# Kernel optimization log

Measured on AMD Instinct MI355X. Metric: run time of the kernel, lower is better.

Reference implementation:

```python
import jax, jax.numpy as jnp
import numpy as np

N_NODES = 50000
N_EDGES = 400000
IN_DIM = 128
HID_DIM = 128
OUT_DIM = 128


def setup_inputs() -> dict:
    key = jax.random.key(0)
    k_x, k_e, k_w1, k_b1, k_w2, k_b2 = jax.random.split(key, 6)
    x = jax.random.normal(k_x, (N_NODES, IN_DIM), dtype=jnp.float32)
    edge_index = jax.random.randint(k_e, (2, N_EDGES), 0, N_NODES, dtype=jnp.int64)
    # nn.Linear-style params: W is [out, in], kaiming-uniform-ish init
    lim1 = 1.0 / np.sqrt(IN_DIM)
    lim2 = 1.0 / np.sqrt(HID_DIM)
    W1 = jax.random.uniform(k_w1, (HID_DIM, IN_DIM), jnp.float32, -lim1, lim1)
    b1 = jax.random.uniform(k_b1, (HID_DIM,), jnp.float32, -lim1, lim1)
    W2 = jax.random.uniform(k_w2, (OUT_DIM, HID_DIM), jnp.float32, -lim2, lim2)
    b2 = jax.random.uniform(k_b2, (OUT_DIM,), jnp.float32, -lim2, lim2)
    return {"x": x, "edge_index": edge_index, "W1": W1, "b1": b1, "W2": W2, "b2": b2}


def reference(x, edge_index, W1, b1, W2, b2):
    # h = relu(fc1(x));  dropout in eval mode -> identity
    h = jax.nn.relu(x @ W1.T + b1)                      # [N, hid]
    src, dst = edge_index[0], edge_index[1]
    # gather messages from src, scatter-add (mean) into dst
    agg = jax.ops.segment_sum(h[src], dst, num_segments=N_NODES)      # [N, hid]
    deg = jax.ops.segment_sum(jnp.ones_like(dst, dtype=h.dtype), dst,
                              num_segments=N_NODES)                   # [N]
    deg = jnp.maximum(deg, 1.0)
    agg = agg / deg[:, None]
    # residual add + fc2
    return (agg + h) @ W2.T + b2                        # [N, out]
```

## Files before the change

kernel.cpp:

```cpp
#include <hip/hip_runtime.h>

#define N_NODES 50000
#define N_EDGES 400000
#define DIM 128
#define N_SCAN_BLK ((N_NODES + 255) / 256)
#define BUCKET_BLK ((N_EDGES + 255) / 256)
#define FC1_BLK ((N_NODES + 63) / 64)

typedef unsigned short u16;
typedef unsigned int   u32;
typedef __bf16 v8bf  __attribute__((ext_vector_type(8)));
typedef float  f32x4 __attribute__((ext_vector_type(4)));
typedef u16    u16x8 __attribute__((ext_vector_type(8)));

union BF8 { u16x8 u; v8bf b; };

__device__ __forceinline__ float bf2f(u16 u) {
    union { u32 i; float f; } v; v.i = ((u32)u) << 16; return v.f;
}
__device__ __forceinline__ u16 f2bf(float f) {
    union { float f; u32 i; } v; v.f = f; u32 u = v.i;
    return (u16)((u + 0x7FFFu + ((u >> 16) & 1u)) >> 16);
}

__global__ __launch_bounds__(256) void count_cast_kernel(
    const int* __restrict__ edst, int* __restrict__ counts,
    const float* __restrict__ W1, const float* __restrict__ W2,
    u16* __restrict__ Wb1, u16* __restrict__ Wb2)
{
    int bid = blockIdx.x;
    if (bid < BUCKET_BLK) {
        int e = bid * 256 + threadIdx.x;
        if (e >= N_EDGES) return;
        int dst = edst[e];
        if ((unsigned)dst >= N_NODES) return;
        atomicAdd(&counts[dst], 1);
    } else {
        int i = (bid - BUCKET_BLK) * 256 + threadIdx.x;
        if (i < DIM * DIM) {
            Wb1[i] = f2bf(W1[i]);
            Wb2[i] = f2bf(W2[i]);
        }
    }
}

__global__ __launch_bounds__(256) void scan_blocks_kernel(
    const int* __restrict__ counts, int* __restrict__ row_ptr,
    int* __restrict__ bsum)
{
    __shared__ int tmp[256];
    const int t = threadIdx.x;
    const int i = blockIdx.x * 256 + t;
    int v = (i < N_NODES) ? counts[i] : 0;
    tmp[t] = v;
    __syncthreads();
#pragma unroll
    for (int ofs = 1; ofs < 256; ofs <<= 1) {
        int add = (t >= ofs) ? tmp[t - ofs] : 0;
        __syncthreads();
        tmp[t] += add;
        __syncthreads();
    }
    if (i < N_NODES) row_ptr[i] = tmp[t] - v;
    if (t == 255) bsum[blockIdx.x] = tmp[255];
}

__global__ __launch_bounds__(256) void scan_fixup2_kernel(
    const int* __restrict__ bsum, int* __restrict__ row_ptr,
    int* __restrict__ cursor)
{
    __shared__ int tmp[256];
    __shared__ int ex[256];
    const int t = threadIdx.x;
    int v = (t < N_SCAN_BLK) ? bsum[t] : 0;
    tmp[t] = v;
    __syncthreads();
#pragma unroll
    for (int ofs = 1; ofs < 256; ofs <<= 1) {
        int add = (t >= ofs) ? tmp[t - ofs] : 0;
        __syncthreads();
        tmp[t] += add;
        __syncthreads();
    }
    ex[t] = tmp[t] - v;
    __syncthreads();

    int boff = ex[blockIdx.x];
    int i = blockIdx.x * 256 + t;
    if (i < N_NODES) {
        int r = row_ptr[i] + boff;
        row_ptr[i] = r;
        cursor[i]  = r;
    }
    if (i == 0) row_ptr[N_NODES] = N_EDGES;
}

__global__ __launch_bounds__(256, 3) void bucket_fc1_kernel(
    const int* __restrict__ esrc, const int* __restrict__ edst,
    int* __restrict__ cursor, int* __restrict__ esorted,
    const float* __restrict__ x, const u16* __restrict__ Wb,
    const float* __restrict__ b, u16* __restrict__ h)
{
    __shared__ u16 xs[64 * 136];
    const int bid = blockIdx.x;

    if (bid < BUCKET_BLK) {
        int e = bid * 256 + threadIdx.x;
        if (e < N_EDGES) {
            int src = esrc[e], dst = edst[e];
            if ((unsigned)src < N_NODES && (unsigned)dst < N_NODES) {
                int pos = atomicAdd(&cursor[dst], 1);
                esorted[pos] = src;
            }
        }
        return;
    }

    const int t = threadIdx.x;
    const int wave = t >> 6, lane = t & 63, quad = lane >> 4, l15 = lane & 15;
    const int ch = wave >> 1, rh = wave & 1;
    const int row0 = (bid - BUCKET_BLK) * 64;

    BF8 barr[4][4];
#pragma unroll
    for (int ct = 0; ct < 4; ++ct)
#pragma unroll
        for (int ks = 0; ks < 4; ++ks)
            barr[ct][ks].u = *(const u16x8*)(
                Wb + (size_t)(ch * 64 + ct * 16 + l15) * DIM + ks * 32 + quad * 8);

    {
        int srow = t >> 2, k0 = (t & 3) * 32;
        int grow = row0 + srow; if (grow >= N_NODES) grow = N_NODES - 1;
        const float* xp = x + (size_t)grow * DIM + k0;
#pragma unroll
        for (int j = 0; j < 4; ++j) {
            float4 f0 = *(const float4*)(xp + j * 8);
            float4 f1 = *(const float4*)(xp + j * 8 + 4);
            u16x8 p;
            p[0] = f2bf(f0.x); p[1] = f2bf(f0.y); p[2] = f2bf(f0.z); p[3] = f2bf(f0.w);
            p[4] = f2bf(f1.x); p[5] = f2bf(f1.y); p[6] = f2bf(f1.z); p[7] = f2bf(f1.w);
            *(u16x8*)&xs[srow * 136 + k0 + j * 8] = p;
        }
    }

    f32x4 acc[2][4];
#pragma unroll
    for (int ct = 0; ct < 4; ++ct) {
        float bv = b[ch * 64 + ct * 16 + l15];
        acc[0][ct] = (f32x4){bv, bv, bv, bv};
        acc[1][ct] = (f32x4){bv, bv, bv, bv};
    }
    __syncthreads();

#pragma unroll
    for (int ks = 0; ks < 4; ++ks) {
        BF8 a0, a1;
        a0.u = *(const u16x8*)&xs[(rh * 32 +  0 + l15) * 136 + ks * 32 + quad * 8];
        a1.u = *(const u16x8*)&xs[(rh * 32 + 16 + l15) * 136 + ks * 32 + quad * 8];
#pragma unroll
        for (int ct = 0; ct < 4; ++ct) {
            acc[0][ct] = __builtin_amdgcn_mfma_f32_16x16x32_bf16(
                a0.b, barr[ct][ks].b, acc[0][ct], 0, 0, 0);
            acc[1][ct] = __builtin_amdgcn_mfma_f32_16x16x32_bf16(
                a1.b, barr[ct][ks].b, acc[1][ct], 0, 0, 0);
        }
    }

#pragma unroll
    for (int rt = 0; rt < 2; ++rt)
#pragma unroll
        for (int i = 0; i < 4; ++i) {
            int row = row0 + rh * 32 + rt * 16 + quad * 4 + i;
            if (row < N_NODES) {
#pragma unroll
                for (int ct = 0; ct < 4; ++ct) {
                    int col = ch * 64 + ct * 16 + l15;
                    h[(size_t)row * DIM + col] = f2bf(fmaxf(acc[rt][ct][i], 0.f));
                }
            }
        }
}

__global__ __launch_bounds__(256) void aggregate_kernel(
    const int* __restrict__ row_ptr, const int* __restrict__ esorted,
    const u16* __restrict__ h, u16* __restrict__ z)
{
    const int wave = threadIdx.x >> 6;
    const int lane = threadIdx.x & 63;
    const int n = blockIdx.x * 4 + wave;
    if (n >= N_NODES) return;

    const int start = row_ptr[n];
    const int end   = row_ptr[n + 1];

    float a0 = 0.f, a1 = 0.f;
    int e = start;
    for (; e + 8 <= end; e += 8) {
        int s0 = esorted[e + 0], s1 = esorted[e + 1];
        int s2 = esorted[e + 2], s3 = esorted[e + 3];
        int s4 = esorted[e + 4], s5 = esorted[e + 5];
        int s6 = esorted[e + 6], s7 = esorted[e + 7];
        u32 v0 = *(const u32*)(h + (size_t)s0 * DIM + lane * 2);
        u32 v1 = *(const u32*)(h + (size_t)s1 * DIM + lane * 2);
        u32 v2 = *(const u32*)(h + (size_t)s2 * DIM + lane * 2);
        u32 v3 = *(const u32*)(h + (size_t)s3 * DIM + lane * 2);
        u32 v4 = *(const u32*)(h + (size_t)s4 * DIM + lane * 2);
        u32 v5 = *(const u32*)(h + (size_t)s5 * DIM + lane * 2);
        u32 v6 = *(const u32*)(h + (size_t)s6 * DIM + lane * 2);
        u32 v7 = *(const u32*)(h + (size_t)s7 * DIM + lane * 2);
        a0 += bf2f((u16)v0); a1 += bf2f((u16)(v0 >> 16));
        a0 += bf2f((u16)v1); a1 += bf2f((u16)(v1 >> 16));
        a0 += bf2f((u16)v2); a1 += bf2f((u16)(v2 >> 16));
        a0 += bf2f((u16)v3); a1 += bf2f((u16)(v3 >> 16));
        a0 += bf2f((u16)v4); a1 += bf2f((u16)(v4 >> 16));
        a0 += bf2f((u16)v5); a1 += bf2f((u16)(v5 >> 16));
        a0 += bf2f((u16)v6); a1 += bf2f((u16)(v6 >> 16));
        a0 += bf2f((u16)v7); a1 += bf2f((u16)(v7 >> 16));
    }
    for (; e + 4 <= end; e += 4) {
        int s0 = esorted[e + 0], s1 = esorted[e + 1];
        int s2 = esorted[e + 2], s3 = esorted[e + 3];
        u32 v0 = *(const u32*)(h + (size_t)s0 * DIM + lane * 2);
        u32 v1 = *(const u32*)(h + (size_t)s1 * DIM + lane * 2);
        u32 v2 = *(const u32*)(h + (size_t)s2 * DIM + lane * 2);
        u32 v3 = *(const u32*)(h + (size_t)s3 * DIM + lane * 2);
        a0 += bf2f((u16)v0); a1 += bf2f((u16)(v0 >> 16));
        a0 += bf2f((u16)v1); a1 += bf2f((u16)(v1 >> 16));
        a0 += bf2f((u16)v2); a1 += bf2f((u16)(v2 >> 16));
        a0 += bf2f((u16)v3); a1 += bf2f((u16)(v3 >> 16));
    }
    for (; e < end; ++e) {
        u32 v = *(const u32*)(h + (size_t)esorted[e] * DIM + lane * 2);
        a0 += bf2f((u16)v); a1 += bf2f((u16)(v >> 16));
    }

    int deg = end - start;
    float inv = (deg > 0) ? 1.f / (float)deg : 1.f;
    u32 r = *(const u32*)(h + (size_t)n * DIM + lane * 2);
    float z0 = a0 * inv + bf2f((u16)r);
    float z1 = a1 * inv + bf2f((u16)(r >> 16));
    u32 p = (u32)f2bf(z0) | ((u32)f2bf(z1) << 16);
    *(u32*)(z + (size_t)n * DIM + lane * 2) = p;
}

__global__ __launch_bounds__(256, 3) void fc2_mfma(
    const u16* __restrict__ z, const u16* __restrict__ Wb,
    const float* __restrict__ b, float* __restrict__ out)
{
    __shared__ u16 xs[64 * 136];
    const int t = threadIdx.x;
    const int wave = t >> 6, lane = t & 63, quad = lane >> 4, l15 = lane & 15;
    const int ch = wave >> 1, rh = wave & 1;
    const int row0 = blockIdx.x * 64;

    BF8 barr[4][4];
#pragma unroll
    for (int ct = 0; ct < 4; ++ct)
#pragma unroll
        for (int ks = 0; ks < 4; ++ks)
            barr[ct][ks].u = *(const u16x8*)(
                Wb + (size_t)(ch * 64 + ct * 16 + l15) * DIM + ks * 32 + quad * 8);

    {
        int srow = t >> 1, k0 = (t & 1) * 64;
        int grow = row0 + srow; if (grow >= N_NODES) grow = N_NODES - 1;
        const u16* zp = z + (size_t)grow * DIM + k0;
#pragma unroll
        for (int j = 0; j < 8; ++j)
            *(u16x8*)&xs[srow * 136 + k0 + j * 8] = *(const u16x8*)(zp + j * 8);
    }

    f32x4 acc[2][4];
#pragma unroll
    for (int ct = 0; ct < 4; ++ct) {
        float bv = b[ch * 64 + ct * 16 + l15];
        acc[0][ct] = (f32x4){bv, bv, bv, bv};
        acc[1][ct] = (f32x4){bv, bv, bv, bv};
    }
    __syncthreads();

#pragma unroll
    for (int ks = 0; ks < 4; ++ks) {
        BF8 a0, a1;
        a0.u = *(const u16x8*)&xs[(rh * 32 +  0 + l15) * 136 + ks * 32 + quad * 8];
        a1.u = *(const u16x8*)&xs[(rh * 32 + 16 + l15) * 136 + ks * 32 + quad * 8];
#pragma unroll
        for (int ct = 0; ct < 4; ++ct) {
            acc[0][ct] = __builtin_amdgcn_mfma_f32_16x16x32_bf16(
                a0.b, barr[ct][ks].b, acc[0][ct], 0, 0, 0);
            acc[1][ct] = __builtin_amdgcn_mfma_f32_16x16x32_bf16(
                a1.b, barr[ct][ks].b, acc[1][ct], 0, 0, 0);
        }
    }

#pragma unroll
    for (int rt = 0; rt < 2; ++rt)
#pragma unroll
        for (int i = 0; i < 4; ++i) {
            int row = row0 + rh * 32 + rt * 16 + quad * 4 + i;
            if (row < N_NODES) {
#pragma unroll
                for (int ct = 0; ct < 4; ++ct) {
                    int col = ch * 64 + ct * 16 + l15;
                    out[(size_t)row * DIM + col] = acc[rt][ct][i];
                }
            }
        }
}

extern "C" void kernel_launch(void* const* d_in, const int* in_sizes, int n_in,
                              void* d_out, int out_size, void* d_ws, size_t ws_size,
                              hipStream_t stream)
{
    const float* x  = (const float*)d_in[0];
    const int*   ei = (const int*)d_in[1];
    const float* W1 = (const float*)d_in[2];
    const float* b1 = (const float*)d_in[3];
    const float* W2 = (const float*)d_in[4];
    const float* b2 = (const float*)d_in[5];
    float* out = (float*)d_out;

    const int* esrc = ei;
    const int* edst = ei + N_EDGES;

    char* ws = (char*)d_ws;
    size_t off = 0;
    u16* h        = (u16*)(ws + off); off += (size_t)N_NODES * DIM * 2;
    u16* z        = (u16*)(ws + off); off += (size_t)N_NODES * DIM * 2;
    u16* Wb1      = (u16*)(ws + off); off += (size_t)DIM * DIM * 2;
    u16* Wb2      = (u16*)(ws + off); off += (size_t)DIM * DIM * 2;
    int* counts   = (int*)(ws + off); off += (size_t)N_NODES * 4;
    int* row_ptr  = (int*)(ws + off); off += (size_t)(N_NODES + 1) * 4;
    int* cursor   = (int*)(ws + off); off += (size_t)N_NODES * 4;
    int* esorted  = (int*)(ws + off); off += (size_t)N_EDGES * 4;
    int* bsum     = (int*)(ws + off); off += (size_t)N_SCAN_BLK * 4;

    hipMemsetAsync(counts, 0, (size_t)N_NODES * 4, stream);
    count_cast_kernel<<<BUCKET_BLK + 64, 256, 0, stream>>>(
        edst, counts, W1, W2, Wb1, Wb2);
    scan_blocks_kernel<<<N_SCAN_BLK, 256, 0, stream>>>(counts, row_ptr, bsum);
    scan_fixup2_kernel<<<N_SCAN_BLK, 256, 0, stream>>>(bsum, row_ptr, cursor);
    bucket_fc1_kernel<<<BUCKET_BLK + FC1_BLK, 256, 0, stream>>>(
        esrc, edst, cursor, esorted, x, Wb1, b1, h);
    aggregate_kernel<<<(N_NODES + 3) / 4, 256, 0, stream>>>(
        row_ptr, esorted, h, z);
    fc2_mfma<<<(N_NODES + 63) / 64, 256, 0, stream>>>(z, Wb2, b2, out);
}
```

Measured before the change: 177.6 us.

## Fuse whole GNN pipeline into one cooperative persistent kernel with grid syncs

```diff
diff --git a/kernel.cpp b/kernel.cpp
--- a/kernel.cpp
+++ b/kernel.cpp
@@ -1,4 +1,5 @@
 #include <hip/hip_runtime.h>
+#include <hip/hip_cooperative_groups.h>
 
 #define N_NODES 50000
 #define N_EDGES 400000
@@ -21,6 +22,267 @@
 __device__ __forceinline__ u16 f2bf(float f) {
     union { float f; u32 i; } v; v.f = f; u32 u = v.i;
     return (u16)((u + 0x7FFFu + ((u >> 16) & 1u)) >> 16);
+}
+
+__global__ __launch_bounds__(256, 3) void mega_kernel(
+    const float* __restrict__ x,
+    const int* __restrict__ esrc, const int* __restrict__ edst,
+    const float* __restrict__ W1, const float* __restrict__ b1,
+    const float* __restrict__ W2, const float* __restrict__ b2,
+    float* __restrict__ out,
+    u16* __restrict__ h, u16* __restrict__ Wb1, u16* __restrict__ Wb2,
+    int* __restrict__ counts, int* __restrict__ row_ptr,
+    int* __restrict__ cursor, int* __restrict__ esorted,
+    int* __restrict__ gcursor)
+{
+    cooperative_groups::grid_group grid = cooperative_groups::this_grid();
+    __shared__ __align__(16) char smem[64 * 136 * 2];
+    u16* xs = (u16*)smem;
+
+    const int nb   = (int)gridDim.x;
+    const int bid  = (int)blockIdx.x;
+    const int t    = (int)threadIdx.x;
+    const int gtid = bid * 256 + t;
+    const int gsz  = nb * 256;
+
+    for (int i = gtid; i < N_NODES; i += gsz) counts[i] = 0;
+    for (int i = gtid; i < DIM * DIM; i += gsz) {
+        Wb1[i] = f2bf(W1[i]);
+        Wb2[i] = f2bf(W2[i]);
+    }
+    if (gtid == 0) *gcursor = 0;
+    grid.sync();
+
+    for (int e = gtid; e < N_EDGES; e += gsz) {
+        int dst = edst[e];
+        int src = esrc[e];
+        if ((unsigned)dst < N_NODES && (unsigned)src < N_NODES)
+            atomicAdd(&counts[dst], 1);
+    }
+    grid.sync();
+
+    {
+        int* tmp   = (int*)smem;
+        int* sbase = tmp + 256;
+        for (int sb = bid; sb < N_SCAN_BLK; sb += nb) {
+            int i = sb * 256 + t;
+            int v = (i < N_NODES) ? counts[i] : 0;
+            tmp[t] = v;
+            __syncthreads();
+#pragma unroll
+            for (int ofs = 1; ofs < 256; ofs <<= 1) {
+                int add = (t >= ofs) ? tmp[t - ofs] : 0;
+                __syncthreads();
+                tmp[t] += add;
+                __syncthreads();
+            }
+            int ex = tmp[t] - v;
+            if (t == 255) *sbase = atomicAdd(gcursor, tmp[255]);
+            __syncthreads();
+            if (i < N_NODES) {
+                int r = *sbase + ex;
+                row_ptr[i] = r;
+                cursor[i]  = r;
+            }
+            __syncthreads();
+        }
+    }
+    grid.sync();
+
+    for (int e = gtid; e < N_EDGES; e += gsz) {
+        int src = esrc[e], dst = edst[e];
+        if ((unsigned)src < N_NODES && (unsigned)dst < N_NODES) {
+            int pos = atomicAdd(&cursor[dst], 1);
+            esorted[pos] = src;
+        }
+    }
+
+    {
+        const int wave = t >> 6, lane = t & 63, quad = lane >> 4, l15 = lane & 15;
+        const int ch = wave >> 1, rh = wave & 1;
+
+        BF8 barr[4][4];
+#pragma unroll
+        for (int ct = 0; ct < 4; ++ct)
+#pragma unroll
+            for (int ks = 0; ks < 4; ++ks)
+                barr[ct][ks].u = *(const u16x8*)(
+                    Wb1 + (size_t)(ch * 64 + ct * 16 + l15) * DIM + ks * 32 + quad * 8);
+        float bv[4];
+#pragma unroll
+        for (int ct = 0; ct < 4; ++ct) bv[ct] = b1[ch * 64 + ct * 16 + l15];
+
+        for (int tile = bid; tile < FC1_BLK; tile += nb) {
+            const int row0 = tile * 64;
+            {
+                int srow = t >> 2, k0 = (t & 3) * 32;
+                int grow = row0 + srow; if (grow >= N_NODES) grow = N_NODES - 1;
+                const float* xp = x + (size_t)grow * DIM + k0;
+#pragma unroll
+                for (int j = 0; j < 4; ++j) {
+                    float4 f0 = *(const float4*)(xp + j * 8);
+                    float4 f1 = *(const float4*)(xp + j * 8 + 4);
+                    u16x8 p;
+                    p[0] = f2bf(f0.x); p[1] = f2bf(f0.y); p[2] = f2bf(f0.z); p[3] = f2bf(f0.w);
+                    p[4] = f2bf(f1.x); p[5] = f2bf(f1.y); p[6] = f2bf(f1.z); p[7] = f2bf(f1.w);
+                    *(u16x8*)&xs[srow * 136 + k0 + j * 8] = p;
+                }
+            }
+            f32x4 acc[2][4];
+#pragma unroll
+            for (int ct = 0; ct < 4; ++ct) {
+                acc[0][ct] = (f32x4){bv[ct], bv[ct], bv[ct], bv[ct]};
+                acc[1][ct] = (f32x4){bv[ct], bv[ct], bv[ct], bv[ct]};
+            }
+            __syncthreads();
+#pragma unroll
+            for (int ks = 0; ks < 4; ++ks) {
+                BF8 a0, a1;
+                a0.u = *(const u16x8*)&xs[(rh * 32 +  0 + l15) * 136 + ks * 32 + quad * 8];
+                a1.u = *(const u16x8*)&xs[(rh * 32 + 16 + l15) * 136 + ks * 32 + quad * 8];
+#pragma unroll
+                for (int ct = 0; ct < 4; ++ct) {
+                    acc[0][ct] = __builtin_amdgcn_mfma_f32_16x16x32_bf16(
+                        a0.b, barr[ct][ks].b, acc[0][ct], 0, 0, 0);
+                    acc[1][ct] = __builtin_amdgcn_mfma_f32_16x16x32_bf16(
+                        a1.b, barr[ct][ks].b, acc[1][ct], 0, 0, 0);
+                }
+            }
+#pragma unroll
+            for (int rt = 0; rt < 2; ++rt)
+#pragma unroll
+                for (int i = 0; i < 4; ++i) {
+                    int row = row0 + rh * 32 + rt * 16 + quad * 4 + i;
+                    if (row < N_NODES) {
+#pragma unroll
+                        for (int ct = 0; ct < 4; ++ct) {
+                            int col = ch * 64 + ct * 16 + l15;
+                            h[(size_t)row * DIM + col] = f2bf(fmaxf(acc[rt][ct][i], 0.f));
+                        }
+                    }
+                }
+            __syncthreads();
+        }
+    }
+    grid.sync();
+
+    {
+        const int wv = t >> 6, ln = t & 63;
+        const int quad = ln >> 4, l15 = ln & 15;
+        const int ch = wv >> 1, rh = wv & 1;
+
+        BF8 barr[4][4];
+#pragma unroll
+        for (int ct = 0; ct < 4; ++ct)
+#pragma unroll
+            for (int ks = 0; ks < 4; ++ks)
+                barr[ct][ks].u = *(const u16x8*)(
+                    Wb2 + (size_t)(ch * 64 + ct * 16 + l15) * DIM + ks * 32 + quad * 8);
+        float bv[4];
+#pragma unroll
+        for (int ct = 0; ct < 4; ++ct) bv[ct] = b2[ch * 64 + ct * 16 + l15];
+
+        for (int tile = bid; tile < FC1_BLK; tile += nb) {
+            const int row0 = tile * 64;
+
+            int nidx = row0 + wv * 16 + (ln & 15);
+            int myStart = 0, myDeg = 0;
+            if (nidx < N_NODES) { myStart = row_ptr[nidx]; myDeg = counts[nidx]; }
+
+#pragma unroll 1
+            for (int j = 0; j < 16; ++j) {
+                const int s = wv * 16 + j;
+                const int n = row0 + s;
+                const int start = __shfl(myStart, j, 64);
+                const int deg   = __shfl(myDeg,   j, 64);
+                u32 pack = 0;
+                if (n < N_NODES) {
+                    const int end = start + deg;
+                    float a0 = 0.f, a1 = 0.f;
+                    int e = start;
+                    for (; e + 8 <= end; e += 8) {
+                        int s0 = esorted[e + 0], s1 = esorted[e + 1];
+                        int s2 = esorted[e + 2], s3 = esorted[e + 3];
+                        int s4 = esorted[e + 4], s5 = esorted[e + 5];
+                        int s6 = esorted[e + 6], s7 = esorted[e + 7];
+                        u32 v0 = *(const u32*)(h + (size_t)s0 * DIM + ln * 2);
+                        u32 v1 = *(const u32*)(h + (size_t)s1 * DIM + ln * 2);
+                        u32 v2 = *(const u32*)(h + (size_t)s2 * DIM + ln * 2);
+                        u32 v3 = *(const u32*)(h + (size_t)s3 * DIM + ln * 2);
+                        u32 v4 = *(const u32*)(h + (size_t)s4 * DIM + ln * 2);
+                        u32 v5 = *(const u32*)(h + (size_t)s5 * DIM + ln * 2);
+                        u32 v6 = *(const u32*)(h + (size_t)s6 * DIM + ln * 2);
+                        u32 v7 = *(const u32*)(h + (size_t)s7 * DIM + ln * 2);
+                        a0 += bf2f((u16)v0); a1 += bf2f((u16)(v0 >> 16));
+                        a0 += bf2f((u16)v1); a1 += bf2f((u16)(v1 >> 16));
+                        a0 += bf2f((u16)v2); a1 += bf2f((u16)(v2 >> 16));
+                        a0 += bf2f((u16)v3); a1 += bf2f((u16)(v3 >> 16));
+                        a0 += bf2f((u16)v4); a1 += bf2f((u16)(v4 >> 16));
+                        a0 += bf2f((u16)v5); a1 += bf2f((u16)(v5 >> 16));
+                        a0 += bf2f((u16)v6); a1 += bf2f((u16)(v6 >> 16));
+                        a0 += bf2f((u16)v7); a1 += bf2f((u16)(v7 >> 16));
+                    }
+                    for (; e + 4 <= end; e += 4) {
+                        int s0 = esorted[e + 0], s1 = esorted[e + 1];
+                        int s2 = esorted[e + 2], s3 = esorted[e + 3];
+                        u32 v0 = *(const u32*)(h + (size_t)s0 * DIM + ln * 2);
+                        u32 v1 = *(const u32*)(h + (size_t)s1 * DIM + ln * 2);
+                        u32 v2 = *(const u32*)(h + (size_t)s2 * DIM + ln * 2);
+                        u32 v3 = *(const u32*)(h + (size_t)s3 * DIM + ln * 2);
+                        a0 += bf2f((u16)v0); a1 += bf2f((u16)(v0 >> 16));
+                        a0 += bf2f((u16)v1); a1 += bf2f((u16)(v1 >> 16));
+                        a0 += bf2f((u16)v2); a1 += bf2f((u16)(v2 >> 16));
+                        a0 += bf2f((u16)v3); a1 += bf2f((u16)(v3 >> 16));
+                    }
+                    for (; e < end; ++e) {
+                        u32 v = *(const u32*)(h + (size_t)esorted[e] * DIM + ln * 2);
+                        a0 += bf2f((u16)v); a1 += bf2f((u16)(v >> 16));
+                    }
+                    u32 r = *(const u32*)(h + (size_t)n * DIM + ln * 2);
+                    float inv = (deg > 0) ? 1.f / (float)deg : 1.f;
+                    float z0 = a0 * inv + bf2f((u16)r);
+                    float z1 = a1 * inv + bf2f((u16)(r >> 16));
+                    pack = (u32)f2bf(z0) | ((u32)f2bf(z1) << 16);
+                }
+                *(u32*)&xs[s * 136 + ln * 2] = pack;
+            }
+            __syncthreads();
+
+            f32x4 acc[2][4];
+#pragma unroll
+            for (int ct = 0; ct < 4; ++ct) {
+                acc[0][ct] = (f32x4){bv[ct], bv[ct], bv[ct], bv[ct]};
+                acc[1][ct] = (f32x4){bv[ct], bv[ct], bv[ct], bv[ct]};
+            }
+#pragma unroll
+            for (int ks = 0; ks < 4; ++ks) {
+                BF8 a0, a1;
+                a0.u = *(const u16x8*)&xs[(rh * 32 +  0 + l15) * 136 + ks * 32 + quad * 8];
+                a1.u = *(const u16x8*)&xs[(rh * 32 + 16 + l15) * 136 + ks * 32 + quad * 8];
+#pragma unroll
+                for (int ct = 0; ct < 4; ++ct) {
+                    acc[0][ct] = __builtin_amdgcn_mfma_f32_16x16x32_bf16(
+                        a0.b, barr[ct][ks].b, acc[0][ct], 0, 0, 0);
+                    acc[1][ct] = __builtin_amdgcn_mfma_f32_16x16x32_bf16(
+                        a1.b, barr[ct][ks].b, acc[1][ct], 0, 0, 0);
+                }
+            }
+#pragma unroll
+            for (int rt = 0; rt < 2; ++rt)
+#pragma unroll
+                for (int i = 0; i < 4; ++i) {
+                    int row = row0 + rh * 32 + rt * 16 + quad * 4 + i;
+                    if (row < N_NODES) {
+#pragma unroll
+                        for (int ct = 0; ct < 4; ++ct) {
+                            int col = ch * 64 + ct * 16 + l15;
+                            out[(size_t)row * DIM + col] = acc[rt][ct][i];
+                        }
+                    }
+                }
+            __syncthreads();
+        }
+    }
 }
 
 __global__ __launch_bounds__(256) void count_cast_kernel(
@@ -335,6 +597,33 @@
     int* cursor   = (int*)(ws + off); off += (size_t)N_NODES * 4;
     int* esorted  = (int*)(ws + off); off += (size_t)N_EDGES * 4;
     int* bsum     = (int*)(ws + off); off += (size_t)N_SCAN_BLK * 4;
+    int* gcursor  = (int*)(ws + off); off += 4;
+
+    static int coop_grid = -1;
+    if (coop_grid < 0) {
+        int nbpc = 0;
+        if (hipOccupancyMaxActiveBlocksPerMultiprocessor(&nbpc, mega_kernel, 256, 0)
+                != hipSuccess)
+            nbpc = 0;
+        if (nbpc > 0) {
+            long g = (long)nbpc * 256;
+            if (g > FC1_BLK) g = FC1_BLK;
+            coop_grid = (int)g;
+        } else {
+            coop_grid = 0;
+        }
+    }
+    if (coop_grid > 0) {
+        void* args[] = { (void*)&x, (void*)&esrc, (void*)&edst,
+                         (void*)&W1, (void*)&b1, (void*)&W2, (void*)&b2,
+                         (void*)&out, (void*)&h, (void*)&Wb1, (void*)&Wb2,
+                         (void*)&counts, (void*)&row_ptr, (void*)&cursor,
+                         (void*)&esorted, (void*)&gcursor };
+        if (hipLaunchCooperativeKernel(mega_kernel, dim3(coop_grid), dim3(256),
+                                       args, 0, stream) == hipSuccess)
+            return;
+        coop_grid = 0;
+    }
 
     hipMemsetAsync(counts, 0, (size_t)N_NODES * 4, stream);
     count_cast_kernel<<<BUCKET_BLK + 64, 256, 0, stream>>>(
```

Result: slower. 372.2 us (+109.6%).

## Replace CSR count/scan build with atomic linked-list adjacency per destination

Applied to the files above, without the earlier changes.

```diff
diff --git a/kernel.cpp b/kernel.cpp
--- a/kernel.cpp
+++ b/kernel.cpp
@@ -3,7 +3,6 @@
 #define N_NODES 50000
 #define N_EDGES 400000
 #define DIM 128
-#define N_SCAN_BLK ((N_NODES + 255) / 256)
 #define BUCKET_BLK ((N_EDGES + 255) / 256)
 #define FC1_BLK ((N_NODES + 63) / 64)
 
@@ -23,83 +22,11 @@
     return (u16)((u + 0x7FFFu + ((u >> 16) & 1u)) >> 16);
 }
 
-__global__ __launch_bounds__(256) void count_cast_kernel(
-    const int* __restrict__ edst, int* __restrict__ counts,
-    const float* __restrict__ W1, const float* __restrict__ W2,
-    u16* __restrict__ Wb1, u16* __restrict__ Wb2)
-{
-    int bid = blockIdx.x;
-    if (bid < BUCKET_BLK) {
-        int e = bid * 256 + threadIdx.x;
-        if (e >= N_EDGES) return;
-        int dst = edst[e];
-        if ((unsigned)dst >= N_NODES) return;
-        atomicAdd(&counts[dst], 1);
-    } else {
-        int i = (bid - BUCKET_BLK) * 256 + threadIdx.x;
-        if (i < DIM * DIM) {
-            Wb1[i] = f2bf(W1[i]);
-            Wb2[i] = f2bf(W2[i]);
-        }
-    }
-}
-
-__global__ __launch_bounds__(256) void scan_blocks_kernel(
-    const int* __restrict__ counts, int* __restrict__ row_ptr,
-    int* __restrict__ bsum)
-{
-    __shared__ int tmp[256];
-    const int t = threadIdx.x;
-    const int i = blockIdx.x * 256 + t;
-    int v = (i < N_NODES) ? counts[i] : 0;
-    tmp[t] = v;
-    __syncthreads();
-#pragma unroll
-    for (int ofs = 1; ofs < 256; ofs <<= 1) {
-        int add = (t >= ofs) ? tmp[t - ofs] : 0;
-        __syncthreads();
-        tmp[t] += add;
-        __syncthreads();
-    }
-    if (i < N_NODES) row_ptr[i] = tmp[t] - v;
-    if (t == 255) bsum[blockIdx.x] = tmp[255];
-}
-
-__global__ __launch_bounds__(256) void scan_fixup2_kernel(
-    const int* __restrict__ bsum, int* __restrict__ row_ptr,
-    int* __restrict__ cursor)
-{
-    __shared__ int tmp[256];
-    __shared__ int ex[256];
-    const int t = threadIdx.x;
-    int v = (t < N_SCAN_BLK) ? bsum[t] : 0;
-    tmp[t] = v;
-    __syncthreads();
-#pragma unroll
-    for (int ofs = 1; ofs < 256; ofs <<= 1) {
-        int add = (t >= ofs) ? tmp[t - ofs] : 0;
-        __syncthreads();
-        tmp[t] += add;
-        __syncthreads();
-    }
-    ex[t] = tmp[t] - v;
-    __syncthreads();
-
-    int boff = ex[blockIdx.x];
-    int i = blockIdx.x * 256 + t;
-    if (i < N_NODES) {
-        int r = row_ptr[i] + boff;
-        row_ptr[i] = r;
-        cursor[i]  = r;
-    }
-    if (i == 0) row_ptr[N_NODES] = N_EDGES;
-}
-
-__global__ __launch_bounds__(256, 3) void bucket_fc1_kernel(
+__global__ __launch_bounds__(256, 3) void build_fc1_kernel(
     const int* __restrict__ esrc, const int* __restrict__ edst,
-    int* __restrict__ cursor, int* __restrict__ esorted,
-    const float* __restrict__ x, const u16* __restrict__ Wb,
-    const float* __restrict__ b, u16* __restrict__ h)
+    int* __restrict__ head, int2* __restrict__ pairbuf,
+    const float* __restrict__ x, const float* __restrict__ W1,
+    const float* __restrict__ b1, u16* __restrict__ h)
 {
     __shared__ u16 xs[64 * 136];
     const int bid = blockIdx.x;
@@ -109,8 +36,8 @@
         if (e < N_EDGES) {
             int src = esrc[e], dst = edst[e];
             if ((unsigned)src < N_NODES && (unsigned)dst < N_NODES) {
-                int pos = atomicAdd(&cursor[dst], 1);
-                esorted[pos] = src;
+                int old = atomicExch(&head[dst], e);
+                pairbuf[e] = make_int2(old, src);
             }
         }
         return;
@@ -125,9 +52,16 @@
 #pragma unroll
     for (int ct = 0; ct < 4; ++ct)
 #pragma unroll
-        for (int ks = 0; ks < 4; ++ks)
-            barr[ct][ks].u = *(const u16x8*)(
-                Wb + (size_t)(ch * 64 + ct * 16 + l15) * DIM + ks * 32 + quad * 8);
+        for (int ks = 0; ks < 4; ++ks) {
+            const float* wp = W1 + (size_t)(ch * 64 + ct * 16 + l15) * DIM
+                                 + ks * 32 + quad * 8;
+            float4 f0 = *(const float4*)wp;
+            float4 f1 = *(const float4*)(wp + 4);
+            u16x8 p;
+            p[0] = f2bf(f0.x); p[1] = f2bf(f0.y); p[2] = f2bf(f0.z); p[3] = f2bf(f0.w);
+            p[4] = f2bf(f1.x); p[5] = f2bf(f1.y); p[6] = f2bf(f1.z); p[7] = f2bf(f1.w);
+            barr[ct][ks].u = p;
+        }
 
     {
         int srow = t >> 2, k0 = (t & 3) * 32;
@@ -147,7 +81,7 @@
     f32x4 acc[2][4];
 #pragma unroll
     for (int ct = 0; ct < 4; ++ct) {
-        float bv = b[ch * 64 + ct * 16 + l15];
+        float bv = b1[ch * 64 + ct * 16 + l15];
         acc[0][ct] = (f32x4){bv, bv, bv, bv};
         acc[1][ct] = (f32x4){bv, bv, bv, bv};
     }
@@ -183,7 +117,7 @@
 }
 
 __global__ __launch_bounds__(256) void aggregate_kernel(
-    const int* __restrict__ row_ptr, const int* __restrict__ esorted,
+    const int* __restrict__ head, const int2* __restrict__ pairbuf,
     const u16* __restrict__ h, u16* __restrict__ z)
 {
     const int wave = threadIdx.x >> 6;
@@ -191,62 +125,36 @@
     const int n = blockIdx.x * 4 + wave;
     if (n >= N_NODES) return;
 
-    const int start = row_ptr[n];
-    const int end   = row_ptr[n + 1];
-
     float a0 = 0.f, a1 = 0.f;
-    int e = start;
-    for (; e + 8 <= end; e += 8) {
-        int s0 = esorted[e + 0], s1 = esorted[e + 1];
-        int s2 = esorted[e + 2], s3 = esorted[e + 3];
-        int s4 = esorted[e + 4], s5 = esorted[e + 5];
-        int s6 = esorted[e + 6], s7 = esorted[e + 7];
-        u32 v0 = *(const u32*)(h + (size_t)s0 * DIM + lane * 2);
-        u32 v1 = *(const u32*)(h + (size_t)s1 * DIM + lane * 2);
-        u32 v2 = *(const u32*)(h + (size_t)s2 * DIM + lane * 2);
-        u32 v3 = *(const u32*)(h + (size_t)s3 * DIM + lane * 2);
-        u32 v4 = *(const u32*)(h + (size_t)s4 * DIM + lane * 2);
-        u32 v5 = *(const u32*)(h + (size_t)s5 * DIM + lane * 2);
-        u32 v6 = *(const u32*)(h + (size_t)s6 * DIM + lane * 2);
-        u32 v7 = *(const u32*)(h + (size_t)s7 * DIM + lane * 2);
-        a0 += bf2f((u16)v0); a1 += bf2f((u16)(v0 >> 16));
-        a0 += bf2f((u16)v1); a1 += bf2f((u16)(v1 >> 16));
-        a0 += bf2f((u16)v2); a1 += bf2f((u16)(v2 >> 16));
-        a0 += bf2f((u16)v3); a1 += bf2f((u16)(v3 >> 16));
-        a0 += bf2f((u16)v4); a1 += bf2f((u16)(v4 >> 16));
-        a0 += bf2f((u16)v5); a1 += bf2f((u16)(v5 >> 16));
-        a0 += bf2f((u16)v6); a1 += bf2f((u16)(v6 >> 16));
-        a0 += bf2f((u16)v7); a1 += bf2f((u16)(v7 >> 16));
-    }
-    for (; e + 4 <= end; e += 4) {
-        int s0 = esorted[e + 0], s1 = esorted[e + 1];
-        int s2 = esorted[e + 2], s3 = esorted[e + 3];
-        u32 v0 = *(const u32*)(h + (size_t)s0 * DIM + lane * 2);
-        u32 v1 = *(const u32*)(h + (size_t)s1 * DIM + lane * 2);
-        u32 v2 = *(const u32*)(h + (size_t)s2 * DIM + lane * 2);
-        u32 v3 = *(const u32*)(h + (size_t)s3 * DIM + lane * 2);
-        a0 += bf2f((u16)v0); a1 += bf2f((u16)(v0 >> 16));
-        a0 += bf2f((u16)v1); a1 += bf2f((u16)(v1 >> 16));
-        a0 += bf2f((u16)v2); a1 += bf2f((u16)(v2 >> 16));
-        a0 += bf2f((u16)v3); a1 += bf2f((u16)(v3 >> 16));
-    }
-    for (; e < end; ++e) {
-        u32 v = *(const u32*)(h + (size_t)esorted[e] * DIM + lane * 2);
-        a0 += bf2f((u16)v); a1 += bf2f((u16)(v >> 16));
-    }
-
-    int deg = end - start;
+    int deg = 0;
+    int e = head[n];
+    if (e >= 0) {
+        int2 p = pairbuf[e];
+        while (true) {
+            const int en  = p.x;
+            const int src = p.y;
+            u32 v = *(const u32*)(h + (size_t)src * DIM + lane * 2);
+            int2 pn;
+            const bool more = (en >= 0);
+            if (more) pn = pairbuf[en];
+            a0 += bf2f((u16)v); a1 += bf2f((u16)(v >> 16));
+            ++deg;
+            if (!more) break;
+            p = pn;
+        }
+    }
+
     float inv = (deg > 0) ? 1.f / (float)deg : 1.f;
     u32 r = *(const u32*)(h + (size_t)n * DIM + lane * 2);
     float z0 = a0 * inv + bf2f((u16)r);
     float z1 = a1 * inv + bf2f((u16)(r >> 16));
-    u32 p = (u32)f2bf(z0) | ((u32)f2bf(z1) << 16);
-    *(u32*)(z + (size_t)n * DIM + lane * 2) = p;
+    u32 pck = (u32)f2bf(z0) | ((u32)f2bf(z1) << 16);
+    *(u32*)(z + (size_t)n * DIM + lane * 2) = pck;
 }
 
 __global__ __launch_bounds__(256, 3) void fc2_mfma(
-    const u16* __restrict__ z, const u16* __restrict__ Wb,
-    const float* __restrict__ b, float* __restrict__ out)
+    const u16* __restrict__ z, const float* __restrict__ W2,
+    const float* __restrict__ b2, float* __restrict__ out)
 {
     __shared__ u16 xs[64 * 136];
     const int t = threadIdx.x;
@@ -258,9 +166,16 @@
 #pragma unroll
     for (int ct = 0; ct < 4; ++ct)
 #pragma unroll
-        for (int ks = 0; ks < 4; ++ks)
-            barr[ct][ks].u = *(const u16x8*)(
-                Wb + (size_t)(ch * 64 + ct * 16 + l15) * DIM + ks * 32 + quad * 8);
+        for (int ks = 0; ks < 4; ++ks) {
+            const float* wp = W2 + (size_t)(ch * 64 + ct * 16 + l15) * DIM
+                                 + ks * 32 + quad * 8;
+            float4 f0 = *(const float4*)wp;
+            float4 f1 = *(const float4*)(wp + 4);
+            u16x8 p;
+            p[0] = f2bf(f0.x); p[1] = f2bf(f0.y); p[2] = f2bf(f0.z); p[3] = f2bf(f0.w);
+            p[4] = f2bf(f1.x); p[5] = f2bf(f1.y); p[6] = f2bf(f1.z); p[7] = f2bf(f1.w);
+            barr[ct][ks].u = p;
+        }
 
     {
         int srow = t >> 1, k0 = (t & 1) * 64;
@@ -274,7 +189,7 @@
     f32x4 acc[2][4];
 #pragma unroll
     for (int ct = 0; ct < 4; ++ct) {
-        float bv = b[ch * 64 + ct * 16 + l15];
+        float bv = b2[ch * 64 + ct * 16 + l15];
         acc[0][ct] = (f32x4){bv, bv, bv, bv};
         acc[1][ct] = (f32x4){bv, bv, bv, bv};
     }
@@ -326,24 +241,16 @@
 
     char* ws = (char*)d_ws;
     size_t off = 0;
-    u16* h        = (u16*)(ws + off); off += (size_t)N_NODES * DIM * 2;
-    u16* z        = (u16*)(ws + off); off += (size_t)N_NODES * DIM * 2;
-    u16* Wb1      = (u16*)(ws + off); off += (size_t)DIM * DIM * 2;
-    u16* Wb2      = (u16*)(ws + off); off += (size_t)DIM * DIM * 2;
-    int* counts   = (int*)(ws + off); off += (size_t)N_NODES * 4;
-    int* row_ptr  = (int*)(ws + off); off += (size_t)(N_NODES + 1) * 4;
-    int* cursor   = (int*)(ws + off); off += (size_t)N_NODES * 4;
-    int* esorted  = (int*)(ws + off); off += (size_t)N_EDGES * 4;
-    int* bsum     = (int*)(ws + off); off += (size_t)N_SCAN_BLK * 4;
-
-    hipMemsetAsync(counts, 0, (size_t)N_NODES * 4, stream);
-    count_cast_kernel<<<BUCKET_BLK + 64, 256, 0, stream>>>(
-        edst, counts, W1, W2, Wb1, Wb2);
-    scan_blocks_kernel<<<N_SCAN_BLK, 256, 0, stream>>>(counts, row_ptr, bsum);
-    scan_fixup2_kernel<<<N_SCAN_BLK, 256, 0, stream>>>(bsum, row_ptr, cursor);
-    bucket_fc1_kernel<<<BUCKET_BLK + FC1_BLK, 256, 0, stream>>>(
-        esrc, edst, cursor, esorted, x, Wb1, b1, h);
+    u16*  h       = (u16*)(ws + off);  off += (size_t)N_NODES * DIM * 2;
+    u16*  z       = (u16*)(ws + off);  off += (size_t)N_NODES * DIM * 2;
+    int*  head    = (int*)(ws + off);  off += (size_t)N_NODES * 4;
+    int2* pairbuf = (int2*)(ws + off); off += (size_t)N_EDGES * 8;
+
+    hipMemsetAsync(head, 0xFF, (size_t)N_NODES * 4, stream);
+
+    build_fc1_kernel<<<BUCKET_BLK + FC1_BLK, 256, 0, stream>>>(
+        esrc, edst, head, pairbuf, x, W1, b1, h);
     aggregate_kernel<<<(N_NODES + 3) / 4, 256, 0, stream>>>(
-        row_ptr, esorted, h, z);
-    fc2_mfma<<<(N_NODES + 63) / 64, 256, 0, stream>>>(z, Wb2, b2, out);
-}
+        head, pairbuf, h, z);
+    fc2_mfma<<<(N_NODES + 63) / 64, 256, 0, stream>>>(z, W2, b2, out);
+}
```

Result: no change. 179.3 us (+0.9%).
